# Performance work log

Measured on AMD Instinct MI355X. Metric: run time of the kernel, lower is better.

Reference implementation:

```python
import jax, jax.numpy as jnp
import numpy as np

B, S, E, H = 16, 512, 4096, 8
HD = E // H  # 512, must equal S for this module's math
LN_EPS = 1e-5
NORM_EPS = 1e-12


def setup_inputs() -> dict:
    key = jax.random.key(0)
    ks = jax.random.split(key, 16)
    s_e = 1.0 / np.sqrt(E)
    s_h = 1.0 / np.sqrt(HD)
    return {
        "x": jax.random.normal(ks[0], (B, S, E), jnp.float32),
        "Wq": jax.random.normal(ks[1], (E, E), jnp.float32) * s_e,
        "bq": jnp.zeros((E,), jnp.float32),
        "Wk": jax.random.normal(ks[2], (E, E), jnp.float32) * s_e,
        "bk": jnp.zeros((E,), jnp.float32),
        "Wv": jax.random.normal(ks[3], (E, E), jnp.float32) * s_e,
        "bv": jnp.zeros((E,), jnp.float32),
        "g_q": jnp.ones((HD,), jnp.float32),
        "b_q": jnp.zeros((HD,), jnp.float32),
        "g_k": jnp.ones((HD,), jnp.float32),
        "b_k": jnp.zeros((HD,), jnp.float32),
        "Wg": jax.random.normal(ks[4], (2 * HD, HD), jnp.float32) * s_h,
        "bg": jnp.zeros((2 * HD,), jnp.float32),
        "Wo": jax.random.normal(ks[5], (E, E), jnp.float32) * s_e,
        "bo": jnp.zeros((E,), jnp.float32),
    }


def _layernorm(t, g, b):
    mu = jnp.mean(t, axis=-1, keepdims=True)
    var = jnp.mean(jnp.square(t - mu), axis=-1, keepdims=True)
    return (t - mu) * jax.lax.rsqrt(var + LN_EPS) * g + b


def reference(x, Wq, bq, Wk, bk, Wv, bv, g_q, b_q, g_k, b_k, Wg, bg, Wo, bo):
    # projections + head split: [B,H,S,HD]
    def proj(W, bias):
        y = jnp.einsum('bse,fe->bsf', x, W) + bias
        return y.reshape(B, S, H, HD).transpose(0, 2, 1, 3)

    q = proj(Wq, bq)
    k = proj(Wk, bk)
    v = proj(Wv, bv)

    # per-head QK LayerNorm over head_dim
    q = _layernorm(q, g_q, b_q)
    k = _layernorm(k, g_k, b_k)

    # scores [B,H,S,S]; note S == HD by construction
    scores = jnp.einsum('bhsd,bhtd->bhst', q, k) / np.sqrt(HD)

    # GeGLU over last dim (linear HD -> 2*HD, chunk, gelu gate)
    h = jnp.einsum('bhst,ft->bhsf', scores, Wg) + bg
    val, gate = h[..., :HD], h[..., HD:]
    w = val * jax.nn.gelu(gate, approximate=False)

    # L2 normalize over last dim (torch F.normalize p=2)
    norm = jnp.sqrt(jnp.sum(jnp.square(w), axis=-1, keepdims=True))
    w = w / jnp.maximum(norm, NORM_EPS)

    # attention-value matmul: [B,H,S,HD] x [B,H,S,HD] with HD==S
    out = jnp.einsum('bhst,bhtd->bhsd', w, v)
    out = out.transpose(0, 2, 1, 3).reshape(B, S, E)
    return jnp.einsum('bse,fe->bsf', out, Wo) + bo
```

## Files before the change

### kernel.cpp

```cpp
#include <hip/hip_runtime.h>
#include <math.h>

#define TILE 128
#define BK 64

typedef __bf16 bf16x8 __attribute__((ext_vector_type(8)));
typedef float f32x4 __attribute__((ext_vector_type(4)));
typedef short short8 __attribute__((ext_vector_type(8)));
typedef unsigned int uint2v __attribute__((ext_vector_type(2)));
typedef unsigned int uint4v __attribute__((ext_vector_type(4)));

__device__ __forceinline__ float bf2f(unsigned short u) {
  union { unsigned int i; float f; } v; v.i = ((unsigned int)u) << 16; return v.f;
}
__device__ __forceinline__ unsigned short f2bf(float f) {
  union { float fl; unsigned int i; } v; v.fl = f;
  unsigned int x = v.i;
  return (unsigned short)((x + 0x7FFFu + ((x >> 16) & 1u)) >> 16);
}
__device__ __forceinline__ unsigned int cvt_pk_bf16(float lo, float hi) {
  unsigned int r;
  asm("v_cvt_pk_bf16_f32 %0, %1, %2" : "=v"(r) : "v"(lo), "v"(hi));
  return r;
}
__device__ __forceinline__ void gl_lds16(const unsigned short* g, void* l) {
  __builtin_amdgcn_global_load_lds(
      (const __attribute__((address_space(1))) unsigned int*)g,
      (__attribute__((address_space(3))) unsigned int*)l, 16, 0, 0);
}

template<int CF32, int HAS_BIAS>
__global__ __launch_bounds__(512)
void gemm256(const unsigned short* __restrict__ A,
             const unsigned short* __restrict__ B,
             const float* __restrict__ bias,
             void* __restrict__ Cv,
             int M, int N, int K, int lda, int ldb, int ldc, int nbn)
{
  __shared__ alignas(16) unsigned char LDS[131072];
  const int NT = K >> 6;

  const int nwg = (int)gridDim.x;
  const int bid = (int)blockIdx.x;
  const int swz = (bid & 7) * (nwg >> 3) + (bid >> 3);
  const int tm = (swz / nbn) * 256;
  const int tn = (swz % nbn) * 256;

  const int tid = (int)threadIdx.x;
  const int lane = tid & 63;
  const int wv = tid >> 6;
  const int wm = wv >> 2;
  const int wn = wv & 3;
  const int l16 = lane & 15;
  const int kg = lane >> 4;

  const int srow = tid >> 3;
  const int scolb = ((tid & 7) * 16) ^ (((tid >> 3) & 7) << 4);
  const unsigned short* Abase = A + (long)tm * lda + (scolb >> 1);
  const unsigned short* Bbase = B + (long)tn * ldb + (scolb >> 1);
  const int ldsw = (tid >> 6) * 1024;

  const int colswz0 = (kg * 16) ^ ((l16 & 7) << 4);
  const int colswz1 = (64 + kg * 16) ^ ((l16 & 7) << 4);

  f32x4 acc[8][4];
  #pragma unroll
  for (int i = 0; i < 8; ++i)
    #pragma unroll
    for (int j = 0; j < 4; ++j)
      #pragma unroll
      for (int e = 0; e < 4; ++e) acc[i][j][e] = 0.f;

  auto stageA = [&](int t) {
    const int buf = t & 1;
    #pragma unroll
    for (int h = 0; h < 2; ++h)
      #pragma unroll
      for (int i = 0; i < 2; ++i)
        gl_lds16(Abase + (long)(h * 128 + srow + i * 64) * lda + t * 64,
                 &LDS[buf * 32768 + h * 16384 + i * 8192 + ldsw]);
  };
  auto stageBh = [&](int t, int h) {
    const int buf = t & 1;
    #pragma unroll
    for (int i = 0; i < 2; ++i)
      gl_lds16(Bbase + (long)(h * 128 + srow + i * 64) * ldb + t * 64,
               &LDS[65536 + buf * 32768 + h * 16384 + i * 8192 + ldsw]);
  };

  stageA(0); stageBh(0, 0); stageBh(0, 1);
  stageA(1); stageBh(1, 0); stageBh(1, 1);
  asm volatile("s_waitcnt vmcnt(8)" ::: "memory");
  __builtin_amdgcn_s_barrier();

  for (int t = 0; t < NT; ++t) {
    const unsigned char* aB = &LDS[(t & 1) * 32768 + wm * 16384];
    const unsigned char* bB = &LDS[65536 + (t & 1) * 32768 + (wn >> 1) * 16384];
    const int brow = (wn & 1) * 64;
    bf16x8 bfrag[4][2];
    #pragma unroll
    for (int j = 0; j < 4; ++j) {
      bf16x8 a0k0 = *(const bf16x8*)(aB + ((2 * j + 0) * 16 + l16) * 128 + colswz0);
      bf16x8 a0k1 = *(const bf16x8*)(aB + ((2 * j + 0) * 16 + l16) * 128 + colswz1);
      bf16x8 a1k0 = *(const bf16x8*)(aB + ((2 * j + 1) * 16 + l16) * 128 + colswz0);
      bf16x8 a1k1 = *(const bf16x8*)(aB + ((2 * j + 1) * 16 + l16) * 128 + colswz1);
      if (j == 0) {
        #pragma unroll
        for (int ni = 0; ni < 4; ++ni) {
          bfrag[ni][0] = *(const bf16x8*)(bB + (brow + ni * 16 + l16) * 128 + colswz0);
          bfrag[ni][1] = *(const bf16x8*)(bB + (brow + ni * 16 + l16) * 128 + colswz1);
        }
        if (t > 0 && t + 1 < NT) stageA(t + 1);
      } else if (j == 1) {
        if (t + 2 < NT) stageBh(t + 2, 0);
      } else if (j == 2) {
        if (t + 2 < NT) stageBh(t + 2, 1);
      }
      __builtin_amdgcn_s_barrier();
      asm volatile("s_waitcnt lgkmcnt(0)" ::: "memory");
      __builtin_amdgcn_sched_barrier(0);
      __builtin_amdgcn_s_setprio(1);
      #pragma unroll
      for (int ni = 0; ni < 4; ++ni) {
        acc[2 * j + 0][ni] = __builtin_amdgcn_mfma_f32_16x16x32_bf16(a0k0, bfrag[ni][0], acc[2 * j + 0][ni], 0, 0, 0);
        acc[2 * j + 0][ni] = __builtin_amdgcn_mfma_f32_16x16x32_bf16(a0k1, bfrag[ni][1], acc[2 * j + 0][ni], 0, 0, 0);
        acc[2 * j + 1][ni] = __builtin_amdgcn_mfma_f32_16x16x32_bf16(a1k0, bfrag[ni][0], acc[2 * j + 1][ni], 0, 0, 0);
        acc[2 * j + 1][ni] = __builtin_amdgcn_mfma_f32_16x16x32_bf16(a1k1, bfrag[ni][1], acc[2 * j + 1][ni], 0, 0, 0);
      }
      __builtin_amdgcn_s_setprio(0);
      if (j == 3) {
        if (t >= NT - 2) { asm volatile("s_waitcnt vmcnt(0)" ::: "memory"); }
        else             { asm volatile("s_waitcnt vmcnt(4)" ::: "memory"); }
        __builtin_amdgcn_sched_barrier(0);
      }
      __builtin_amdgcn_s_barrier();
    }
  }

  const int crow0 = tm + wm * 128 + kg * 4;
  const int ccol0 = tn + wn * 64 + l16;
  #pragma unroll
  for (int ni = 0; ni < 4; ++ni) {
    const int col = ccol0 + ni * 16;
    const float bv = HAS_BIAS ? bias[col] : 0.f;
    #pragma unroll
    for (int mi = 0; mi < 8; ++mi) {
      #pragma unroll
      for (int jj = 0; jj < 4; ++jj) {
        const int row = crow0 + mi * 16 + jj;
        const float v = acc[mi][ni][jj] + bv;
        if (CF32) ((float*)Cv)[(long)row * ldc + col] = v;
        else ((unsigned short*)Cv)[(long)row * ldc + col] = f2bf(v);
      }
    }
  }
}

__global__ __launch_bounds__(256)
void cvt_bf16(const float* __restrict__ in, unsigned short* __restrict__ out, long n8)
{
  long i = (long)blockIdx.x * 256 + threadIdx.x;
  const long stride = (long)gridDim.x * 256;
  for (; i < n8; i += stride) {
    f32x4 v0 = *(const f32x4*)(in + i * 8);
    f32x4 v1 = *(const f32x4*)(in + i * 8 + 4);
    uint4v o;
    o[0] = cvt_pk_bf16(v0[0], v0[1]);
    o[1] = cvt_pk_bf16(v0[2], v0[3]);
    o[2] = cvt_pk_bf16(v1[0], v1[1]);
    o[3] = cvt_pk_bf16(v1[2], v1[3]);
    *(uint4v*)(out + i * 8) = o;
  }
}

template<int HAS_BIAS>
__global__ __launch_bounds__(256, 2)
void gemm_bt(const unsigned short* __restrict__ A, const unsigned short* __restrict__ B,
             const float* __restrict__ bias, unsigned short* __restrict__ C,
             int M, int N, int K, int lda, int ldb, int ldc,
             long sAo, long sAi, int nAi,
             long sBo, long sBi, int nBi,
             long sCo, long sCi, int nCi,
             float alpha)
{
  __shared__ alignas(16) unsigned short lA[TILE * BK];
  __shared__ alignas(16) unsigned short lB[TILE * BK];

  const int z = blockIdx.z;
  const unsigned short* Ab = A + (long)(z / nAi) * sAo + (long)(z % nAi) * sAi;
  const unsigned short* Bb = B + (long)(z / nBi) * sBo + (long)(z % nBi) * sBi;
  unsigned short* Cb = C + (long)(z / nCi) * sCo + (long)(z % nCi) * sCi;

  const int tm = blockIdx.y * TILE;
  const int tn = blockIdx.x * TILE;
  const int tid = (int)threadIdx.x;
  const int lane = tid & 63;
  const int wave = tid >> 6;
  const int wm = (wave >> 1) * 64;
  const int wn = (wave & 1) * 64;
  const int l16 = lane & 15;
  const int kg = lane >> 4;

  f32x4 acc[4][4];
  #pragma unroll
  for (int i = 0; i < 4; ++i)
    #pragma unroll
    for (int j = 0; j < 4; ++j)
      #pragma unroll
      for (int e = 0; e < 4; ++e) acc[i][j][e] = 0.f;

  const int srow = tid >> 3;
  const int sc8 = (tid & 7) * 8;
  const int fbA = (wm + l16) * BK + kg * 8;
  const int fbB = (wn + l16) * BK + kg * 8;

  for (int k0 = 0; k0 < K; k0 += BK) {
    short8 ra[4], rb[4];
    #pragma unroll
    for (int i = 0; i < 4; ++i) {
      ra[i] = *(const short8*)(Ab + (long)(tm + srow + i * 32) * lda + k0 + sc8);
      rb[i] = *(const short8*)(Bb + (long)(tn + srow + i * 32) * ldb + k0 + sc8);
    }
    __syncthreads();
    #pragma unroll
    for (int i = 0; i < 4; ++i) {
      *(short8*)&lA[(srow + i * 32) * BK + sc8] = ra[i];
      *(short8*)&lB[(srow + i * 32) * BK + sc8] = rb[i];
    }
    __syncthreads();
    #pragma unroll
    for (int kk = 0; kk < 2; ++kk) {
      bf16x8 af[4], bfr[4];
      #pragma unroll
      for (int mi = 0; mi < 4; ++mi)
        af[mi] = *(const bf16x8*)&lA[fbA + mi * 16 * BK + kk * 32];
      #pragma unroll
      for (int ni = 0; ni < 4; ++ni)
        bfr[ni] = *(const bf16x8*)&lB[fbB + ni * 16 * BK + kk * 32];
      #pragma unroll
      for (int mi = 0; mi < 4; ++mi)
        #pragma unroll
        for (int ni = 0; ni < 4; ++ni)
          acc[mi][ni] = __builtin_amdgcn_mfma_f32_16x16x32_bf16(af[mi], bfr[ni], acc[mi][ni], 0, 0, 0);
    }
  }

  #pragma unroll
  for (int ni = 0; ni < 4; ++ni) {
    int col = tn + wn + ni * 16 + l16;
    float bv = HAS_BIAS ? bias[col] : 0.f;
    #pragma unroll
    for (int mi = 0; mi < 4; ++mi)
      #pragma unroll
      for (int j = 0; j < 4; ++j) {
        int row = tm + wm + mi * 16 + kg * 4 + j;
        Cb[(long)row * ldc + col] = f2bf(acc[mi][ni][j] * alpha + bv);
      }
  }
}

__global__ __launch_bounds__(256)
void ln_rows(unsigned short* __restrict__ t, const float* __restrict__ g,
             const float* __restrict__ b)
{
  const int row = blockIdx.x * 4 + ((int)threadIdx.x >> 6);
  const int lane = (int)threadIdx.x & 63;
  unsigned short* p = t + (long)row * 512 + lane * 8;
  short8 rv = *(const short8*)p;
  float x[8];
  #pragma unroll
  for (int j = 0; j < 8; ++j) x[j] = bf2f((unsigned short)rv[j]);
  float s = 0.f;
  #pragma unroll
  for (int j = 0; j < 8; ++j) s += x[j];
  #pragma unroll
  for (int off = 32; off > 0; off >>= 1) s += __shfl_xor(s, off, 64);
  float mu = s * (1.f / 512.f);
  float vs = 0.f;
  #pragma unroll
  for (int j = 0; j < 8; ++j) { float d = x[j] - mu; vs += d * d; }
  #pragma unroll
  for (int off = 32; off > 0; off >>= 1) vs += __shfl_xor(vs, off, 64);
  float rs = rsqrtf(vs * (1.f / 512.f) + 1e-5f);
  f32x4 gv0 = *(const f32x4*)(g + lane * 8);
  f32x4 gv1 = *(const f32x4*)(g + lane * 8 + 4);
  f32x4 bv0 = *(const f32x4*)(b + lane * 8);
  f32x4 bv1 = *(const f32x4*)(b + lane * 8 + 4);
  short8 ov;
  #pragma unroll
  for (int j = 0; j < 4; ++j) ov[j] = (short)f2bf((x[j] - mu) * rs * gv0[j] + bv0[j]);
  #pragma unroll
  for (int j = 0; j < 4; ++j) ov[4 + j] = (short)f2bf((x[4 + j] - mu) * rs * gv1[j] + bv1[j]);
  *(short8*)p = ov;
}

__global__ __launch_bounds__(256)
void gate_norm(const unsigned short* __restrict__ h, unsigned short* __restrict__ w)
{
  const int row = blockIdx.x * 4 + ((int)threadIdx.x >> 6);
  const int lane = (int)threadIdx.x & 63;
  const unsigned short* hp = h + (long)row * 1024 + lane * 8;
  short8 vv = *(const short8*)hp;
  short8 gg = *(const short8*)(hp + 512);
  float wv[8];
  float ssq = 0.f;
  #pragma unroll
  for (int j = 0; j < 8; ++j) {
    float val = bf2f((unsigned short)vv[j]);
    float gt  = bf2f((unsigned short)gg[j]);
    float tt  = val * (0.5f * gt * (1.f + erff(gt * 0.70710678118654752f)));
    wv[j] = tt;
    ssq += tt * tt;
  }
  #pragma unroll
  for (int off = 32; off > 0; off >>= 1) ssq += __shfl_xor(ssq, off, 64);
  float scale = 1.f / fmaxf(sqrtf(ssq), 1e-12f);
  short8 ov;
  #pragma unroll
  for (int j = 0; j < 8; ++j) ov[j] = (short)f2bf(wv[j] * scale);
  *(short8*)(w + (long)row * 512 + lane * 8) = ov;
}

__global__ __launch_bounds__(256)
void transpose_v(const unsigned short* __restrict__ v, unsigned short* __restrict__ vT)
{
  __shared__ alignas(16) unsigned short lt[64][72];
  const int bh = blockIdx.z;
  const int b = bh >> 3, hh = bh & 7;
  const int d0 = blockIdx.x * 64, t0 = blockIdx.y * 64;
  const int tid = (int)threadIdx.x;
  const unsigned short* src = v + (long)b * (512L * 4096L) + hh * 512;
  #pragma unroll
  for (int it = 0; it < 2; ++it) {
    int ci = it * 256 + tid;
    int r = ci >> 3, c8 = (ci & 7) * 8;
    *(short8*)&lt[r][c8] = *(const short8*)(src + (long)(t0 + r) * 4096 + d0 + c8);
  }
  __syncthreads();
  unsigned short* dst = vT + ((long)bh * 512 + d0) * 512 + t0;
  #pragma unroll
  for (int it = 0; it < 2; ++it) {
    int ci = it * 256 + tid;
    int rr = ci >> 3, c8 = (ci & 7) * 8;
    short8 o;
    #pragma unroll
    for (int j = 0; j < 8; ++j) o[j] = (short)lt[c8 + j][rr];
    *(short8*)(dst + (long)rr * 512 + c8) = o;
  }
}

extern "C" void kernel_launch(void* const* d_in, const int* in_sizes, int n_in,
                              void* d_out, int out_size, void* d_ws, size_t ws_size,
                              hipStream_t stream)
{
  (void)in_sizes; (void)n_in; (void)out_size; (void)ws_size;
  const float* x   = (const float*)d_in[0];
  const float* Wq  = (const float*)d_in[1];
  const float* bq  = (const float*)d_in[2];
  const float* Wk  = (const float*)d_in[3];
  const float* bk  = (const float*)d_in[4];
  const float* Wv  = (const float*)d_in[5];
  const float* bv  = (const float*)d_in[6];
  const float* g_q = (const float*)d_in[7];
  const float* b_q = (const float*)d_in[8];
  const float* g_k = (const float*)d_in[9];
  const float* b_k = (const float*)d_in[10];
  const float* Wg  = (const float*)d_in[11];
  const float* bg  = (const float*)d_in[12];
  const float* Wo  = (const float*)d_in[13];
  const float* bo  = (const float*)d_in[14];
  float* out = (float*)d_out;

  const long NE  = 33554432L;
  const long NE2 = NE / 2;
  unsigned short* ws    = (unsigned short*)d_ws;
  unsigned short* xb    = ws;
  unsigned short* Wslot = ws + NE;
  unsigned short* qbuf  = ws + NE + NE2;
  unsigned short* kbuf  = ws + 2 * NE + NE2;
  unsigned short* vbuf  = ws + 3 * NE + NE2;
  unsigned short* Wob   = ws + 4 * NE + NE2;
  unsigned short* Wgb   = ws + 5 * NE;
  unsigned short* sbuf  = xb;
  unsigned short* vT    = qbuf;
  unsigned short* hbuf  = kbuf;
  unsigned short* wbuf  = xb;
  unsigned short* obuf  = kbuf;

  dim3 blk256(256), blk512(512);
  const float inv_sqrt_hd = 0.044194173824159216f;

  cvt_bf16<<<16384, blk256, 0, stream>>>(x, xb, NE / 8);
  cvt_bf16<<<256, blk256, 0, stream>>>(Wg, Wgb, 524288L / 8);
  cvt_bf16<<<8192, blk256, 0, stream>>>(Wo, Wob, NE2 / 8);

  cvt_bf16<<<8192, blk256, 0, stream>>>(Wq, Wslot, NE2 / 8);
  gemm256<0, 1><<<512, blk512, 0, stream>>>(xb, Wslot, bq, qbuf,
      8192, 4096, 4096, 4096, 4096, 4096, 16);
  cvt_bf16<<<8192, blk256, 0, stream>>>(Wk, Wslot, NE2 / 8);
  gemm256<0, 1><<<512, blk512, 0, stream>>>(xb, Wslot, bk, kbuf,
      8192, 4096, 4096, 4096, 4096, 4096, 16);
  cvt_bf16<<<8192, blk256, 0, stream>>>(Wv, Wslot, NE2 / 8);
  gemm256<0, 1><<<512, blk512, 0, stream>>>(xb, Wslot, bv, vbuf,
      8192, 4096, 4096, 4096, 4096, 4096, 16);

  ln_rows<<<16384, blk256, 0, stream>>>(qbuf, g_q, b_q);
  ln_rows<<<16384, blk256, 0, stream>>>(kbuf, g_k, b_k);

  gemm_bt<0><<<dim3(4, 4, 128), blk256, 0, stream>>>(qbuf, kbuf, nullptr, sbuf,
      512, 512, 512, 4096, 4096, 512,
      2097152L, 512L, 8, 2097152L, 512L, 8, 262144L, 0L, 1, inv_sqrt_hd);

  transpose_v<<<dim3(8, 8, 128), blk256, 0, stream>>>(vbuf, vT);

  gemm_bt<1><<<dim3(8, 4, 128), blk256, 0, stream>>>(sbuf, Wgb, bg, hbuf,
      512, 1024, 512, 512, 512, 1024,
      262144L, 0L, 1, 0L, 0L, 1, 524288L, 0L, 1, 1.f);

  gate_norm<<<16384, blk256, 0, stream>>>(hbuf, wbuf);

  gemm_bt<0><<<dim3(4, 4, 128), blk256, 0, stream>>>(wbuf, vT, nullptr, obuf,
      512, 512, 512, 512, 512, 4096,
      262144L, 0L, 1, 262144L, 0L, 1, 2097152L, 512L, 8, 1.f);

  gemm256<1, 1><<<512, blk512, 0, stream>>>(obuf, Wob, bo, out,
      8192, 4096, 4096, 4096, 4096, 4096, 16);
}
```

Baseline: 1.450 ms.

## Switch big GEMM to 32x32x16 MFMA with 4x4 supertile block swizzle

The 256x256 GEMM used for the QKV and output projections now computes each wave's 128x64 sub-tile with 32x32x16 bf16 MFMA instead of 16x16x32. This doubles work per instruction and reduces LDS fragment reads per FLOP. The K step is split into two half-phases instead of four quarters, and the A refill and both B-half prefetches are regrouped around them. Block-to-tile mapping now groups workgroups into 4x4 supertiles for better L2 reuse, and the unused M/N arguments are dropped. The epilogue is rewritten for the 32x32 accumulator layout, with a risk of higher register pressure from the larger fragments.

```diff
diff --git a/kernel.cpp b/kernel.cpp
--- a/kernel.cpp
+++ b/kernel.cpp
@@ -6,8 +6,8 @@
 
 typedef __bf16 bf16x8 __attribute__((ext_vector_type(8)));
 typedef float f32x4 __attribute__((ext_vector_type(4)));
+typedef float f32x16 __attribute__((ext_vector_type(16)));
 typedef short short8 __attribute__((ext_vector_type(8)));
-typedef unsigned int uint2v __attribute__((ext_vector_type(2)));
 typedef unsigned int uint4v __attribute__((ext_vector_type(4)));
 
 __device__ __forceinline__ float bf2f(unsigned short u) {
@@ -35,41 +35,41 @@
              const unsigned short* __restrict__ B,
              const float* __restrict__ bias,
              void* __restrict__ Cv,
-             int M, int N, int K, int lda, int ldb, int ldc, int nbn)
+             int K, int lda, int ldb, int ldc, int nbn)
 {
   __shared__ alignas(16) unsigned char LDS[131072];
   const int NT = K >> 6;
 
   const int nwg = (int)gridDim.x;
   const int bid = (int)blockIdx.x;
-  const int swz = (bid & 7) * (nwg >> 3) + (bid >> 3);
-  const int tm = (swz / nbn) * 256;
-  const int tn = (swz % nbn) * 256;
+  const int s = (bid & 7) * (nwg >> 3) + (bid >> 3);
+  const int sTile = s >> 4, w = s & 15;
+  const int snb = nbn >> 2;
+  const int tm = ((sTile / snb) * 4 + (w >> 2)) * 256;
+  const int tn = ((sTile % snb) * 4 + (w & 3)) * 256;
 
   const int tid = (int)threadIdx.x;
   const int lane = tid & 63;
   const int wv = tid >> 6;
   const int wm = wv >> 2;
   const int wn = wv & 3;
-  const int l16 = lane & 15;
-  const int kg = lane >> 4;
+  const int l31 = lane & 31;
+  const int hi16 = ((lane >> 5) << 4);
+  const int swz8 = (lane & 7) << 4;
 
   const int srow = tid >> 3;
   const int scolb = ((tid & 7) * 16) ^ (((tid >> 3) & 7) << 4);
   const unsigned short* Abase = A + (long)tm * lda + (scolb >> 1);
   const unsigned short* Bbase = B + (long)tn * ldb + (scolb >> 1);
-  const int ldsw = (tid >> 6) * 1024;
-
-  const int colswz0 = (kg * 16) ^ ((l16 & 7) << 4);
-  const int colswz1 = (64 + kg * 16) ^ ((l16 & 7) << 4);
-
-  f32x4 acc[8][4];
-  #pragma unroll
-  for (int i = 0; i < 8; ++i)
-    #pragma unroll
-    for (int j = 0; j < 4; ++j)
-      #pragma unroll
-      for (int e = 0; e < 4; ++e) acc[i][j][e] = 0.f;
+  const int ldsw = wv * 1024;
+
+  f32x16 acc[4][2];
+  #pragma unroll
+  for (int i = 0; i < 4; ++i)
+    #pragma unroll
+    for (int j = 0; j < 2; ++j)
+      #pragma unroll
+      for (int e = 0; e < 16; ++e) acc[i][j][e] = 0.f;
 
   auto stageA = [&](int t) {
     const int buf = t & 1;
@@ -97,58 +97,71 @@
     const unsigned char* aB = &LDS[(t & 1) * 32768 + wm * 16384];
     const unsigned char* bB = &LDS[65536 + (t & 1) * 32768 + (wn >> 1) * 16384];
     const int brow = (wn & 1) * 64;
-    bf16x8 bfrag[4][2];
-    #pragma unroll
-    for (int j = 0; j < 4; ++j) {
-      bf16x8 a0k0 = *(const bf16x8*)(aB + ((2 * j + 0) * 16 + l16) * 128 + colswz0);
-      bf16x8 a0k1 = *(const bf16x8*)(aB + ((2 * j + 0) * 16 + l16) * 128 + colswz1);
-      bf16x8 a1k0 = *(const bf16x8*)(aB + ((2 * j + 1) * 16 + l16) * 128 + colswz0);
-      bf16x8 a1k1 = *(const bf16x8*)(aB + ((2 * j + 1) * 16 + l16) * 128 + colswz1);
-      if (j == 0) {
+    bf16x8 afr[2][4], bfr[2][4];
+
+    #pragma unroll
+    for (int rb = 0; rb < 2; ++rb)
+      #pragma unroll
+      for (int ks = 0; ks < 4; ++ks)
+        afr[rb][ks] = *(const bf16x8*)(aB + (rb * 32 + l31) * 128 + ((ks * 32 + hi16) ^ swz8));
+    #pragma unroll
+    for (int nb = 0; nb < 2; ++nb)
+      #pragma unroll
+      for (int ks = 0; ks < 4; ++ks)
+        bfr[nb][ks] = *(const bf16x8*)(bB + (brow + nb * 32 + l31) * 128 + ((ks * 32 + hi16) ^ swz8));
+    if (t > 0 && t + 1 < NT) stageA(t + 1);
+    __builtin_amdgcn_s_barrier();
+    asm volatile("s_waitcnt lgkmcnt(0)" ::: "memory");
+    __builtin_amdgcn_sched_barrier(0);
+    __builtin_amdgcn_s_setprio(1);
+    #pragma unroll
+    for (int rb = 0; rb < 2; ++rb)
+      #pragma unroll
+      for (int nb = 0; nb < 2; ++nb)
         #pragma unroll
-        for (int ni = 0; ni < 4; ++ni) {
-          bfrag[ni][0] = *(const bf16x8*)(bB + (brow + ni * 16 + l16) * 128 + colswz0);
-          bfrag[ni][1] = *(const bf16x8*)(bB + (brow + ni * 16 + l16) * 128 + colswz1);
-        }
-        if (t > 0 && t + 1 < NT) stageA(t + 1);
-      } else if (j == 1) {
-        if (t + 2 < NT) stageBh(t + 2, 0);
-      } else if (j == 2) {
-        if (t + 2 < NT) stageBh(t + 2, 1);
-      }
-      __builtin_amdgcn_s_barrier();
-      asm volatile("s_waitcnt lgkmcnt(0)" ::: "memory");
-      __builtin_amdgcn_sched_barrier(0);
-      __builtin_amdgcn_s_setprio(1);
-      #pragma unroll
-      for (int ni = 0; ni < 4; ++ni) {
-        acc[2 * j + 0][ni] = __builtin_amdgcn_mfma_f32_16x16x32_bf16(a0k0, bfrag[ni][0], acc[2 * j + 0][ni], 0, 0, 0);
-        acc[2 * j + 0][ni] = __builtin_amdgcn_mfma_f32_16x16x32_bf16(a0k1, bfrag[ni][1], acc[2 * j + 0][ni], 0, 0, 0);
-        acc[2 * j + 1][ni] = __builtin_amdgcn_mfma_f32_16x16x32_bf16(a1k0, bfrag[ni][0], acc[2 * j + 1][ni], 0, 0, 0);
-        acc[2 * j + 1][ni] = __builtin_amdgcn_mfma_f32_16x16x32_bf16(a1k1, bfrag[ni][1], acc[2 * j + 1][ni], 0, 0, 0);
-      }
-      __builtin_amdgcn_s_setprio(0);
-      if (j == 3) {
-        if (t >= NT - 2) { asm volatile("s_waitcnt vmcnt(0)" ::: "memory"); }
-        else             { asm volatile("s_waitcnt vmcnt(4)" ::: "memory"); }
-        __builtin_amdgcn_sched_barrier(0);
-      }
-      __builtin_amdgcn_s_barrier();
-    }
-  }
-
-  const int crow0 = tm + wm * 128 + kg * 4;
-  const int ccol0 = tn + wn * 64 + l16;
-  #pragma unroll
-  for (int ni = 0; ni < 4; ++ni) {
-    const int col = ccol0 + ni * 16;
+        for (int ks = 0; ks < 4; ++ks)
+          acc[rb][nb] = __builtin_amdgcn_mfma_f32_32x32x16_bf16(
+              afr[rb][ks], bfr[nb][ks], acc[rb][nb], 0, 0, 0);
+    __builtin_amdgcn_s_setprio(0);
+    __builtin_amdgcn_s_barrier();
+
+    #pragma unroll
+    for (int rb = 0; rb < 2; ++rb)
+      #pragma unroll
+      for (int ks = 0; ks < 4; ++ks)
+        afr[rb][ks] = *(const bf16x8*)(aB + ((2 + rb) * 32 + l31) * 128 + ((ks * 32 + hi16) ^ swz8));
+    if (t + 2 < NT) { stageBh(t + 2, 0); stageBh(t + 2, 1); }
+    __builtin_amdgcn_s_barrier();
+    asm volatile("s_waitcnt lgkmcnt(0)" ::: "memory");
+    __builtin_amdgcn_sched_barrier(0);
+    __builtin_amdgcn_s_setprio(1);
+    #pragma unroll
+    for (int rb = 0; rb < 2; ++rb)
+      #pragma unroll
+      for (int nb = 0; nb < 2; ++nb)
+        #pragma unroll
+        for (int ks = 0; ks < 4; ++ks)
+          acc[2 + rb][nb] = __builtin_amdgcn_mfma_f32_32x32x16_bf16(
+              afr[rb][ks], bfr[nb][ks], acc[2 + rb][nb], 0, 0, 0);
+    __builtin_amdgcn_s_setprio(0);
+    if (t >= NT - 2) { asm volatile("s_waitcnt vmcnt(0)" ::: "memory"); }
+    else             { asm volatile("s_waitcnt vmcnt(4)" ::: "memory"); }
+    __builtin_amdgcn_sched_barrier(0);
+    __builtin_amdgcn_s_barrier();
+  }
+
+  const int r0 = tm + wm * 128 + ((lane >> 5) << 2);
+  const int c0 = tn + wn * 64 + l31;
+  #pragma unroll
+  for (int nb = 0; nb < 2; ++nb) {
+    const int col = c0 + nb * 32;
     const float bv = HAS_BIAS ? bias[col] : 0.f;
     #pragma unroll
-    for (int mi = 0; mi < 8; ++mi) {
-      #pragma unroll
-      for (int jj = 0; jj < 4; ++jj) {
-        const int row = crow0 + mi * 16 + jj;
-        const float v = acc[mi][ni][jj] + bv;
+    for (int mi = 0; mi < 4; ++mi) {
+      #pragma unroll
+      for (int r = 0; r < 16; ++r) {
+        const int row = r0 + mi * 32 + (r & 3) + ((r >> 2) << 3);
+        const float v = acc[mi][nb][r] + bv;
         if (CF32) ((float*)Cv)[(long)row * ldc + col] = v;
         else ((unsigned short*)Cv)[(long)row * ldc + col] = f2bf(v);
       }
@@ -396,13 +409,13 @@
 
   cvt_bf16<<<8192, blk256, 0, stream>>>(Wq, Wslot, NE2 / 8);
   gemm256<0, 1><<<512, blk512, 0, stream>>>(xb, Wslot, bq, qbuf,
-      8192, 4096, 4096, 4096, 4096, 4096, 16);
+      4096, 4096, 4096, 4096, 16);
   cvt_bf16<<<8192, blk256, 0, stream>>>(Wk, Wslot, NE2 / 8);
   gemm256<0, 1><<<512, blk512, 0, stream>>>(xb, Wslot, bk, kbuf,
-      8192, 4096, 4096, 4096, 4096, 4096, 16);
+      4096, 4096, 4096, 4096, 16);
   cvt_bf16<<<8192, blk256, 0, stream>>>(Wv, Wslot, NE2 / 8);
   gemm256<0, 1><<<512, blk512, 0, stream>>>(xb, Wslot, bv, vbuf,
-      8192, 4096, 4096, 4096, 4096, 4096, 16);
+      4096, 4096, 4096, 4096, 16);
 
   ln_rows<<<16384, blk256, 0, stream>>>(qbuf, g_q, b_q);
   ln_rows<<<16384, blk256, 0, stream>>>(kbuf, g_k, b_k);
@@ -424,5 +437,5 @@
       262144L, 0L, 1, 262144L, 0L, 1, 2097152L, 512L, 8, 1.f);
 
   gemm256<1, 1><<<512, blk512, 0, stream>>>(obuf, Wob, bo, out,
-      8192, 4096, 4096, 4096, 4096, 4096, 16);
-}
+      4096, 4096, 4096, 4096, 16);
+}
```

After: 1.498 ms. +3.3%, slower.

## Software-pipeline LDS fragment loads across phases and tile 4x4 blocks for L2 locality

Applied to the files above, without the earlier changes.

Reworks the main 256x256 GEMM loop so A fragments for the next phase and B fragments plus the first A fragment for the next K-tile are read from LDS while the current MFMAs run. It uses partial lgkmcnt waits and double-buffered B fragment registers, and unrolls the K loop by two. It also remaps workgroup IDs into 4x4 super-tiles to improve L2 reuse of A and B panels. This costs more VGPRs and more delicate wait/barrier accounting, and assumes NT is even.

```diff
diff --git a/kernel.cpp b/kernel.cpp
--- a/kernel.cpp
+++ b/kernel.cpp
@@ -7,7 +7,6 @@
 typedef __bf16 bf16x8 __attribute__((ext_vector_type(8)));
 typedef float f32x4 __attribute__((ext_vector_type(4)));
 typedef short short8 __attribute__((ext_vector_type(8)));
-typedef unsigned int uint2v __attribute__((ext_vector_type(2)));
 typedef unsigned int uint4v __attribute__((ext_vector_type(4)));
 
 __device__ __forceinline__ float bf2f(unsigned short u) {
@@ -35,16 +34,18 @@
              const unsigned short* __restrict__ B,
              const float* __restrict__ bias,
              void* __restrict__ Cv,
-             int M, int N, int K, int lda, int ldb, int ldc, int nbn)
+             int K, int lda, int ldb, int ldc, int nbn)
 {
   __shared__ alignas(16) unsigned char LDS[131072];
   const int NT = K >> 6;
 
   const int nwg = (int)gridDim.x;
   const int bid = (int)blockIdx.x;
-  const int swz = (bid & 7) * (nwg >> 3) + (bid >> 3);
-  const int tm = (swz / nbn) * 256;
-  const int tn = (swz % nbn) * 256;
+  const int s = (bid & 7) * (nwg >> 3) + (bid >> 3);
+  const int sTile = s >> 4, w = s & 15;
+  const int snb = nbn >> 2;
+  const int tm = ((sTile / snb) * 4 + (w >> 2)) * 256;
+  const int tn = ((sTile % snb) * 4 + (w & 3)) * 256;
 
   const int tid = (int)threadIdx.x;
   const int lane = tid & 63;
@@ -58,10 +59,12 @@
   const int scolb = ((tid & 7) * 16) ^ (((tid >> 3) & 7) << 4);
   const unsigned short* Abase = A + (long)tm * lda + (scolb >> 1);
   const unsigned short* Bbase = B + (long)tn * ldb + (scolb >> 1);
-  const int ldsw = (tid >> 6) * 1024;
+  const int ldsw = wv * 1024;
 
   const int colswz0 = (kg * 16) ^ ((l16 & 7) << 4);
   const int colswz1 = (64 + kg * 16) ^ ((l16 & 7) << 4);
+  const int bq16 = (wn >> 1) * 16384;
+  const int brow = (wn & 1) * 64;
 
   f32x4 acc[8][4];
   #pragma unroll
@@ -71,8 +74,7 @@
       #pragma unroll
       for (int e = 0; e < 4; ++e) acc[i][j][e] = 0.f;
 
-  auto stageA = [&](int t) {
-    const int buf = t & 1;
+  auto stageA = [&](int t, int buf) {
     #pragma unroll
     for (int h = 0; h < 2; ++h)
       #pragma unroll
@@ -80,74 +82,105 @@
         gl_lds16(Abase + (long)(h * 128 + srow + i * 64) * lda + t * 64,
                  &LDS[buf * 32768 + h * 16384 + i * 8192 + ldsw]);
   };
-  auto stageBh = [&](int t, int h) {
-    const int buf = t & 1;
+  auto stageBh = [&](int t, int h, int buf) {
     #pragma unroll
     for (int i = 0; i < 2; ++i)
       gl_lds16(Bbase + (long)(h * 128 + srow + i * 64) * ldb + t * 64,
                &LDS[65536 + buf * 32768 + h * 16384 + i * 8192 + ldsw]);
   };
 
-  stageA(0); stageBh(0, 0); stageBh(0, 1);
-  stageA(1); stageBh(1, 0); stageBh(1, 1);
+  stageA(0, 0); stageBh(0, 0, 0); stageBh(0, 1, 0);
+  stageA(1, 1); stageBh(1, 0, 1); stageBh(1, 1, 1);
   asm volatile("s_waitcnt vmcnt(8)" ::: "memory");
   __builtin_amdgcn_s_barrier();
 
-  for (int t = 0; t < NT; ++t) {
-    const unsigned char* aB = &LDS[(t & 1) * 32768 + wm * 16384];
-    const unsigned char* bB = &LDS[65536 + (t & 1) * 32768 + (wn >> 1) * 16384];
-    const int brow = (wn & 1) * 64;
-    bf16x8 bfrag[4][2];
-    #pragma unroll
-    for (int j = 0; j < 4; ++j) {
-      bf16x8 a0k0 = *(const bf16x8*)(aB + ((2 * j + 0) * 16 + l16) * 128 + colswz0);
-      bf16x8 a0k1 = *(const bf16x8*)(aB + ((2 * j + 0) * 16 + l16) * 128 + colswz1);
-      bf16x8 a1k0 = *(const bf16x8*)(aB + ((2 * j + 1) * 16 + l16) * 128 + colswz0);
-      bf16x8 a1k1 = *(const bf16x8*)(aB + ((2 * j + 1) * 16 + l16) * 128 + colswz1);
-      if (j == 0) {
-        #pragma unroll
-        for (int ni = 0; ni < 4; ++ni) {
-          bfrag[ni][0] = *(const bf16x8*)(bB + (brow + ni * 16 + l16) * 128 + colswz0);
-          bfrag[ni][1] = *(const bf16x8*)(bB + (brow + ni * 16 + l16) * 128 + colswz1);
-        }
-        if (t > 0 && t + 1 < NT) stageA(t + 1);
-      } else if (j == 1) {
-        if (t + 2 < NT) stageBh(t + 2, 0);
-      } else if (j == 2) {
-        if (t + 2 < NT) stageBh(t + 2, 1);
-      }
-      __builtin_amdgcn_s_barrier();
-      asm volatile("s_waitcnt lgkmcnt(0)" ::: "memory");
-      __builtin_amdgcn_sched_barrier(0);
-      __builtin_amdgcn_s_setprio(1);
-      #pragma unroll
-      for (int ni = 0; ni < 4; ++ni) {
-        acc[2 * j + 0][ni] = __builtin_amdgcn_mfma_f32_16x16x32_bf16(a0k0, bfrag[ni][0], acc[2 * j + 0][ni], 0, 0, 0);
-        acc[2 * j + 0][ni] = __builtin_amdgcn_mfma_f32_16x16x32_bf16(a0k1, bfrag[ni][1], acc[2 * j + 0][ni], 0, 0, 0);
-        acc[2 * j + 1][ni] = __builtin_amdgcn_mfma_f32_16x16x32_bf16(a1k0, bfrag[ni][0], acc[2 * j + 1][ni], 0, 0, 0);
-        acc[2 * j + 1][ni] = __builtin_amdgcn_mfma_f32_16x16x32_bf16(a1k1, bfrag[ni][1], acc[2 * j + 1][ni], 0, 0, 0);
-      }
-      __builtin_amdgcn_s_setprio(0);
-      if (j == 3) {
-        if (t >= NT - 2) { asm volatile("s_waitcnt vmcnt(0)" ::: "memory"); }
-        else             { asm volatile("s_waitcnt vmcnt(4)" ::: "memory"); }
-        __builtin_amdgcn_sched_barrier(0);
-      }
-      __builtin_amdgcn_s_barrier();
-    }
-  }
-
-  const int crow0 = tm + wm * 128 + kg * 4;
-  const int ccol0 = tn + wn * 64 + l16;
+  bf16x8 af[2][2][2];
+  bf16x8 bfE[4][2], bfO[4][2];
+
+#define LOADA(P, RB, BASE)                                                     \
+  af[P][0][0] = *(const bf16x8*)((BASE) + ((RB) * 16 + l16) * 128 + colswz0);  \
+  af[P][0][1] = *(const bf16x8*)((BASE) + ((RB) * 16 + l16) * 128 + colswz1);  \
+  af[P][1][0] = *(const bf16x8*)((BASE) + ((RB + 1) * 16 + l16) * 128 + colswz0); \
+  af[P][1][1] = *(const bf16x8*)((BASE) + ((RB + 1) * 16 + l16) * 128 + colswz1);
+
+#define LOADB(BF, BASE)                                                        \
+  _Pragma("unroll")                                                            \
+  for (int ni = 0; ni < 4; ++ni) {                                             \
+    BF[ni][0] = *(const bf16x8*)((BASE) + (brow + ni * 16 + l16) * 128 + colswz0); \
+    BF[ni][1] = *(const bf16x8*)((BASE) + (brow + ni * 16 + l16) * 128 + colswz1); \
+  }
+
+#define MFMA16(R0, P, BF)                                                      \
+  _Pragma("unroll")                                                            \
+  for (int ni = 0; ni < 4; ++ni) {                                             \
+    acc[R0][ni] = __builtin_amdgcn_mfma_f32_16x16x32_bf16(af[P][0][0], BF[ni][0], acc[R0][ni], 0, 0, 0);         \
+    acc[R0][ni] = __builtin_amdgcn_mfma_f32_16x16x32_bf16(af[P][0][1], BF[ni][1], acc[R0][ni], 0, 0, 0);         \
+    acc[R0 + 1][ni] = __builtin_amdgcn_mfma_f32_16x16x32_bf16(af[P][1][0], BF[ni][0], acc[R0 + 1][ni], 0, 0, 0); \
+    acc[R0 + 1][ni] = __builtin_amdgcn_mfma_f32_16x16x32_bf16(af[P][1][1], BF[ni][1], acc[R0 + 1][ni], 0, 0, 0); \
+  }
+
+#define PHASE_STD(P_LOAD, RB_LOAD, R0, P_USE, BF, EXTRA)                       \
+  LOADA(P_LOAD, RB_LOAD, aB)                                                   \
+  EXTRA                                                                        \
+  asm volatile("s_waitcnt lgkmcnt(4)" ::: "memory");                           \
+  __builtin_amdgcn_sched_barrier(0);                                           \
+  __builtin_amdgcn_s_setprio(1);                                               \
+  MFMA16(R0, P_USE, BF)                                                        \
+  __builtin_amdgcn_s_setprio(0);                                               \
+  __builtin_amdgcn_s_barrier();
+
+#define TILE_BODY(TPAR, BFU, BFN)                                              \
+  {                                                                            \
+    const unsigned char* aB  = &LDS[(TPAR) * 32768 + wm * 16384];              \
+    const unsigned char* naB = &LDS[(1 - (TPAR)) * 32768 + wm * 16384];        \
+    const unsigned char* nbB = &LDS[65536 + (1 - (TPAR)) * 32768 + bq16];      \
+    PHASE_STD(1, 2, 0, 0, BFU, )                                               \
+    PHASE_STD(0, 4, 2, 1, BFU,                                                 \
+              if (t > 0 && t + 1 < NT) stageA(t + 1, 1 - (TPAR));)             \
+    PHASE_STD(1, 6, 4, 0, BFU,                                                 \
+              if (t + 2 < NT) { stageBh(t + 2, 0, TPAR); stageBh(t + 2, 1, TPAR); }) \
+    if (t + 1 < NT) {                                                          \
+      if (t >= NT - 2) { asm volatile("s_waitcnt vmcnt(0)" ::: "memory"); }    \
+      else             { asm volatile("s_waitcnt vmcnt(4)" ::: "memory"); }    \
+      __builtin_amdgcn_s_barrier();                                            \
+      LOADB(BFN, nbB)                                                          \
+      LOADA(0, 0, naB)                                                         \
+      asm volatile("s_waitcnt lgkmcnt(12)" ::: "memory");                      \
+    } else {                                                                   \
+      asm volatile("s_waitcnt lgkmcnt(0)" ::: "memory");                       \
+    }                                                                          \
+    __builtin_amdgcn_sched_barrier(0);                                         \
+    __builtin_amdgcn_s_setprio(1);                                             \
+    MFMA16(6, 1, BFU)                                                          \
+    __builtin_amdgcn_s_setprio(0);                                             \
+  }
+
+  {
+    const unsigned char* aB = &LDS[wm * 16384];
+    const unsigned char* bB = &LDS[65536 + bq16];
+    LOADB(bfE, bB)
+    LOADA(0, 0, aB)
+  }
+
+  for (int t2 = 0; t2 < NT; t2 += 2) {
+    { const int t = t2;     TILE_BODY(0, bfE, bfO) }
+    { const int t = t2 + 1; TILE_BODY(1, bfO, bfE) }
+  }
+#undef LOADA
+#undef LOADB
+#undef MFMA16
+#undef PHASE_STD
+#undef TILE_BODY
+
   #pragma unroll
   for (int ni = 0; ni < 4; ++ni) {
-    const int col = ccol0 + ni * 16;
+    const int col = tn + wn * 64 + ni * 16 + l16;
     const float bv = HAS_BIAS ? bias[col] : 0.f;
     #pragma unroll
     for (int mi = 0; mi < 8; ++mi) {
       #pragma unroll
       for (int jj = 0; jj < 4; ++jj) {
-        const int row = crow0 + mi * 16 + jj;
+        const int row = tm + wm * 128 + mi * 16 + kg * 4 + jj;
         const float v = acc[mi][ni][jj] + bv;
         if (CF32) ((float*)Cv)[(long)row * ldc + col] = v;
         else ((unsigned short*)Cv)[(long)row * ldc + col] = f2bf(v);
@@ -396,13 +429,13 @@
 
   cvt_bf16<<<8192, blk256, 0, stream>>>(Wq, Wslot, NE2 / 8);
   gemm256<0, 1><<<512, blk512, 0, stream>>>(xb, Wslot, bq, qbuf,
-      8192, 4096, 4096, 4096, 4096, 4096, 16);
+      4096, 4096, 4096, 4096, 16);
   cvt_bf16<<<8192, blk256, 0, stream>>>(Wk, Wslot, NE2 / 8);
   gemm256<0, 1><<<512, blk512, 0, stream>>>(xb, Wslot, bk, kbuf,
-      8192, 4096, 4096, 4096, 4096, 4096, 16);
+      4096, 4096, 4096, 4096, 16);
   cvt_bf16<<<8192, blk256, 0, stream>>>(Wv, Wslot, NE2 / 8);
   gemm256<0, 1><<<512, blk512, 0, stream>>>(xb, Wslot, bv, vbuf,
-      8192, 4096, 4096, 4096, 4096, 4096, 16);
+      4096, 4096, 4096, 4096, 16);
 
   ln_rows<<<16384, blk256, 0, stream>>>(qbuf, g_q, b_q);
   ln_rows<<<16384, blk256, 0, stream>>>(kbuf, g_k, b_k);
@@ -424,5 +457,5 @@
       262144L, 0L, 1, 262144L, 0L, 1, 2097152L, 512L, 8, 1.f);
 
   gemm256<1, 1><<<512, blk512, 0, stream>>>(obuf, Wob, bo, out,
-      8192, 4096, 4096, 4096, 4096, 4096, 16);
-}
+      4096, 4096, 4096, 4096, 16);
+}
```

Result: slower. 2.840 ms (+95.9%).

## Fuse QKV projections into one GEMM and use 256-tile kernel for batched GEMMs

Applied to the files above, without the earlier changes.

Concatenates Wq/Wk/Wv into one bf16 weight buffer and runs a single 8192x12288 GEMM that routes each output tile to q, k or v with the matching bias. This removes two launches and the serialized per-weight conversions. The 256x256 pipelined gemm256 gains a batched mode and replaces the older 128-tile gemm_bt for the per-head scores, GeGLU and attention-value GEMMs. The non-batched tile mapping also changes to 4x4 supertile grouping for L2 locality. Batched launches have fewer blocks (512-1024) with large tiles, which may underfill the GPU, and the workspace layout is reshuffled to fit the larger weight buffer.

```diff
diff --git a/kernel.cpp b/kernel.cpp
--- a/kernel.cpp
+++ b/kernel.cpp
@@ -1,13 +1,9 @@
 #include <hip/hip_runtime.h>
 #include <math.h>
-
-#define TILE 128
-#define BK 64
 
 typedef __bf16 bf16x8 __attribute__((ext_vector_type(8)));
 typedef float f32x4 __attribute__((ext_vector_type(4)));
 typedef short short8 __attribute__((ext_vector_type(8)));
-typedef unsigned int uint2v __attribute__((ext_vector_type(2)));
 typedef unsigned int uint4v __attribute__((ext_vector_type(4)));
 
 __device__ __forceinline__ float bf2f(unsigned short u) {
@@ -29,22 +25,40 @@
       (__attribute__((address_space(3))) unsigned int*)l, 16, 0, 0);
 }
 
-template<int CF32, int HAS_BIAS>
+template<int BATCH, int SPLIT3, int CF32, int HAS_BIAS>
 __global__ __launch_bounds__(512)
 void gemm256(const unsigned short* __restrict__ A,
              const unsigned short* __restrict__ B,
-             const float* __restrict__ bias,
-             void* __restrict__ Cv,
-             int M, int N, int K, int lda, int ldb, int ldc, int nbn)
+             const float* __restrict__ b0, const float* __restrict__ b1,
+             const float* __restrict__ b2,
+             void* __restrict__ C0, void* __restrict__ C1, void* __restrict__ C2,
+             int K, int lda, int ldb, int ldc, int nbn, float alpha,
+             long sAo, long sAi, int nAi,
+             long sBo, long sBi, int nBi,
+             long sCo, long sCi, int nCi)
 {
   __shared__ alignas(16) unsigned char LDS[131072];
   const int NT = K >> 6;
 
-  const int nwg = (int)gridDim.x;
-  const int bid = (int)blockIdx.x;
-  const int swz = (bid & 7) * (nwg >> 3) + (bid >> 3);
-  const int tm = (swz / nbn) * 256;
-  const int tn = (swz % nbn) * 256;
+  int tm, tn;
+  long offA = 0, offB = 0, offC = 0;
+  if (BATCH) {
+    const int bx = (int)blockIdx.x;
+    tm = (bx / nbn) * 256;
+    tn = (bx % nbn) * 256;
+    const int z = (int)blockIdx.z;
+    offA = (long)(z / nAi) * sAo + (long)(z % nAi) * sAi;
+    offB = (long)(z / nBi) * sBo + (long)(z % nBi) * sBi;
+    offC = (long)(z / nCi) * sCo + (long)(z % nCi) * sCi;
+  } else {
+    const int nwg = (int)gridDim.x;
+    const int bid = (int)blockIdx.x;
+    const int s = (bid & 7) * (nwg >> 3) + (bid >> 3);
+    const int sTile = s >> 4, w = s & 15;
+    const int snb = nbn >> 2;
+    tm = ((sTile / snb) * 4 + (w >> 2)) * 256;
+    tn = ((sTile % snb) * 4 + (w & 3)) * 256;
+  }
 
   const int tid = (int)threadIdx.x;
   const int lane = tid & 63;
@@ -56,9 +70,9 @@
 
   const int srow = tid >> 3;
   const int scolb = ((tid & 7) * 16) ^ (((tid >> 3) & 7) << 4);
-  const unsigned short* Abase = A + (long)tm * lda + (scolb >> 1);
-  const unsigned short* Bbase = B + (long)tn * ldb + (scolb >> 1);
-  const int ldsw = (tid >> 6) * 1024;
+  const unsigned short* Abase = A + offA + (long)tm * lda + (scolb >> 1);
+  const unsigned short* Bbase = B + offB + (long)tn * ldb + (scolb >> 1);
+  const int ldsw = wv * 1024;
 
   const int colswz0 = (kg * 16) ^ ((l16 & 7) << 4);
   const int colswz1 = (64 + kg * 16) ^ ((l16 & 7) << 4);
@@ -137,20 +151,22 @@
     }
   }
 
-  const int crow0 = tm + wm * 128 + kg * 4;
-  const int ccol0 = tn + wn * 64 + l16;
+  const int which = SPLIT3 ? (tn >> 12) : 0;
+  const float* bp = SPLIT3 ? (which == 0 ? b0 : (which == 1 ? b1 : b2)) : b0;
+  void* Cp = SPLIT3 ? (which == 0 ? C0 : (which == 1 ? C1 : C2)) : C0;
+  const int tnn = SPLIT3 ? (tn & 4095) : tn;
   #pragma unroll
   for (int ni = 0; ni < 4; ++ni) {
-    const int col = ccol0 + ni * 16;
-    const float bv = HAS_BIAS ? bias[col] : 0.f;
+    const int col = tnn + wn * 64 + ni * 16 + l16;
+    const float bv = HAS_BIAS ? bp[col] : 0.f;
     #pragma unroll
     for (int mi = 0; mi < 8; ++mi) {
       #pragma unroll
       for (int jj = 0; jj < 4; ++jj) {
-        const int row = crow0 + mi * 16 + jj;
-        const float v = acc[mi][ni][jj] + bv;
-        if (CF32) ((float*)Cv)[(long)row * ldc + col] = v;
-        else ((unsigned short*)Cv)[(long)row * ldc + col] = f2bf(v);
+        const int row = tm + wm * 128 + mi * 16 + kg * 4 + jj;
+        const float v = acc[mi][ni][jj] * alpha + bv;
+        if (CF32) ((float*)Cp)[offC + (long)row * ldc + col] = v;
+        else ((unsigned short*)Cp)[offC + (long)row * ldc + col] = f2bf(v);
       }
     }
   }
@@ -170,92 +186,6 @@
     o[2] = cvt_pk_bf16(v1[0], v1[1]);
     o[3] = cvt_pk_bf16(v1[2], v1[3]);
     *(uint4v*)(out + i * 8) = o;
-  }
-}
-
-template<int HAS_BIAS>
-__global__ __launch_bounds__(256, 2)
-void gemm_bt(const unsigned short* __restrict__ A, const unsigned short* __restrict__ B,
-             const float* __restrict__ bias, unsigned short* __restrict__ C,
-             int M, int N, int K, int lda, int ldb, int ldc,
-             long sAo, long sAi, int nAi,
-             long sBo, long sBi, int nBi,
-             long sCo, long sCi, int nCi,
-             float alpha)
-{
-  __shared__ alignas(16) unsigned short lA[TILE * BK];
-  __shared__ alignas(16) unsigned short lB[TILE * BK];
-
-  const int z = blockIdx.z;
-  const unsigned short* Ab = A + (long)(z / nAi) * sAo + (long)(z % nAi) * sAi;
-  const unsigned short* Bb = B + (long)(z / nBi) * sBo + (long)(z % nBi) * sBi;
-  unsigned short* Cb = C + (long)(z / nCi) * sCo + (long)(z % nCi) * sCi;
-
-  const int tm = blockIdx.y * TILE;
-  const int tn = blockIdx.x * TILE;
-  const int tid = (int)threadIdx.x;
-  const int lane = tid & 63;
-  const int wave = tid >> 6;
-  const int wm = (wave >> 1) * 64;
-  const int wn = (wave & 1) * 64;
-  const int l16 = lane & 15;
-  const int kg = lane >> 4;
-
-  f32x4 acc[4][4];
-  #pragma unroll
-  for (int i = 0; i < 4; ++i)
-    #pragma unroll
-    for (int j = 0; j < 4; ++j)
-      #pragma unroll
-      for (int e = 0; e < 4; ++e) acc[i][j][e] = 0.f;
-
-  const int srow = tid >> 3;
-  const int sc8 = (tid & 7) * 8;
-  const int fbA = (wm + l16) * BK + kg * 8;
-  const int fbB = (wn + l16) * BK + kg * 8;
-
-  for (int k0 = 0; k0 < K; k0 += BK) {
-    short8 ra[4], rb[4];
-    #pragma unroll
-    for (int i = 0; i < 4; ++i) {
-      ra[i] = *(const short8*)(Ab + (long)(tm + srow + i * 32) * lda + k0 + sc8);
-      rb[i] = *(const short8*)(Bb + (long)(tn + srow + i * 32) * ldb + k0 + sc8);
-    }
-    __syncthreads();
-    #pragma unroll
-    for (int i = 0; i < 4; ++i) {
-      *(short8*)&lA[(srow + i * 32) * BK + sc8] = ra[i];
-      *(short8*)&lB[(srow + i * 32) * BK + sc8] = rb[i];
-    }
-    __syncthreads();
-    #pragma unroll
-    for (int kk = 0; kk < 2; ++kk) {
-      bf16x8 af[4], bfr[4];
-      #pragma unroll
-      for (int mi = 0; mi < 4; ++mi)
-        af[mi] = *(const bf16x8*)&lA[fbA + mi * 16 * BK + kk * 32];
-      #pragma unroll
-      for (int ni = 0; ni < 4; ++ni)
-        bfr[ni] = *(const bf16x8*)&lB[fbB + ni * 16 * BK + kk * 32];
-      #pragma unroll
-      for (int mi = 0; mi < 4; ++mi)
-        #pragma unroll
-        for (int ni = 0; ni < 4; ++ni)
-          acc[mi][ni] = __builtin_amdgcn_mfma_f32_16x16x32_bf16(af[mi], bfr[ni], acc[mi][ni], 0, 0, 0);
-    }
-  }
-
-  #pragma unroll
-  for (int ni = 0; ni < 4; ++ni) {
-    int col = tn + wn + ni * 16 + l16;
-    float bv = HAS_BIAS ? bias[col] : 0.f;
-    #pragma unroll
-    for (int mi = 0; mi < 4; ++mi)
-      #pragma unroll
-      for (int j = 0; j < 4; ++j) {
-        int row = tm + wm + mi * 16 + kg * 4 + j;
-        Cb[(long)row * ldc + col] = f2bf(acc[mi][ni][j] * alpha + bv);
-      }
   }
 }
 
@@ -375,12 +305,12 @@
   const long NE2 = NE / 2;
   unsigned short* ws    = (unsigned short*)d_ws;
   unsigned short* xb    = ws;
-  unsigned short* Wslot = ws + NE;
-  unsigned short* qbuf  = ws + NE + NE2;
-  unsigned short* kbuf  = ws + 2 * NE + NE2;
-  unsigned short* vbuf  = ws + 3 * NE + NE2;
-  unsigned short* Wob   = ws + 4 * NE + NE2;
-  unsigned short* Wgb   = ws + 5 * NE;
+  unsigned short* Wqkv  = ws + NE;
+  unsigned short* qbuf  = ws + NE + 3 * NE2;
+  unsigned short* kbuf  = qbuf + NE;
+  unsigned short* vbuf  = kbuf + NE;
+  unsigned short* Wgb   = Wqkv;
+  unsigned short* Wob   = Wqkv + 524288;
   unsigned short* sbuf  = xb;
   unsigned short* vT    = qbuf;
   unsigned short* hbuf  = kbuf;
@@ -388,41 +318,51 @@
   unsigned short* obuf  = kbuf;
 
   dim3 blk256(256), blk512(512);
-  const float inv_sqrt_hd = 0.044194173824159216f;
+  const float isq = 0.044194173824159216f;
 
   cvt_bf16<<<16384, blk256, 0, stream>>>(x, xb, NE / 8);
+  cvt_bf16<<<8192, blk256, 0, stream>>>(Wq, Wqkv, NE2 / 8);
+  cvt_bf16<<<8192, blk256, 0, stream>>>(Wk, Wqkv + NE2, NE2 / 8);
+  cvt_bf16<<<8192, blk256, 0, stream>>>(Wv, Wqkv + 2 * NE2, NE2 / 8);
+
+  gemm256<0, 1, 0, 1><<<1536, blk512, 0, stream>>>(
+      xb, Wqkv, bq, bk, bv, qbuf, kbuf, vbuf,
+      4096, 4096, 4096, 4096, 48, 1.f,
+      0L, 0L, 1, 0L, 0L, 1, 0L, 0L, 1);
+
   cvt_bf16<<<256, blk256, 0, stream>>>(Wg, Wgb, 524288L / 8);
   cvt_bf16<<<8192, blk256, 0, stream>>>(Wo, Wob, NE2 / 8);
 
-  cvt_bf16<<<8192, blk256, 0, stream>>>(Wq, Wslot, NE2 / 8);
-  gemm256<0, 1><<<512, blk512, 0, stream>>>(xb, Wslot, bq, qbuf,
-      8192, 4096, 4096, 4096, 4096, 4096, 16);
-  cvt_bf16<<<8192, blk256, 0, stream>>>(Wk, Wslot, NE2 / 8);
-  gemm256<0, 1><<<512, blk512, 0, stream>>>(xb, Wslot, bk, kbuf,
-      8192, 4096, 4096, 4096, 4096, 4096, 16);
-  cvt_bf16<<<8192, blk256, 0, stream>>>(Wv, Wslot, NE2 / 8);
-  gemm256<0, 1><<<512, blk512, 0, stream>>>(xb, Wslot, bv, vbuf,
-      8192, 4096, 4096, 4096, 4096, 4096, 16);
-
   ln_rows<<<16384, blk256, 0, stream>>>(qbuf, g_q, b_q);
   ln_rows<<<16384, blk256, 0, stream>>>(kbuf, g_k, b_k);
 
-  gemm_bt<0><<<dim3(4, 4, 128), blk256, 0, stream>>>(qbuf, kbuf, nullptr, sbuf,
-      512, 512, 512, 4096, 4096, 512,
-      2097152L, 512L, 8, 2097152L, 512L, 8, 262144L, 0L, 1, inv_sqrt_hd);
+  gemm256<1, 0, 0, 0><<<dim3(4, 1, 128), blk512, 0, stream>>>(
+      qbuf, kbuf, nullptr, nullptr, nullptr, sbuf, nullptr, nullptr,
+      512, 4096, 4096, 512, 2, isq,
+      2097152L, 512L, 8,
+      2097152L, 512L, 8,
+      262144L, 0L, 1);
 
   transpose_v<<<dim3(8, 8, 128), blk256, 0, stream>>>(vbuf, vT);
 
-  gemm_bt<1><<<dim3(8, 4, 128), blk256, 0, stream>>>(sbuf, Wgb, bg, hbuf,
-      512, 1024, 512, 512, 512, 1024,
-      262144L, 0L, 1, 0L, 0L, 1, 524288L, 0L, 1, 1.f);
+  gemm256<1, 0, 0, 1><<<dim3(8, 1, 128), blk512, 0, stream>>>(
+      sbuf, Wgb, bg, nullptr, nullptr, hbuf, nullptr, nullptr,
+      512, 512, 512, 1024, 4, 1.f,
+      262144L, 0L, 1,
+      0L, 0L, 1,
+      524288L, 0L, 1);
 
   gate_norm<<<16384, blk256, 0, stream>>>(hbuf, wbuf);
 
-  gemm_bt<0><<<dim3(4, 4, 128), blk256, 0, stream>>>(wbuf, vT, nullptr, obuf,
-      512, 512, 512, 512, 512, 4096,
-      262144L, 0L, 1, 262144L, 0L, 1, 2097152L, 512L, 8, 1.f);
-
-  gemm256<1, 1><<<512, blk512, 0, stream>>>(obuf, Wob, bo, out,
-      8192, 4096, 4096, 4096, 4096, 4096, 16);
-}
+  gemm256<1, 0, 0, 0><<<dim3(4, 1, 128), blk512, 0, stream>>>(
+      wbuf, vT, nullptr, nullptr, nullptr, obuf, nullptr, nullptr,
+      512, 512, 512, 4096, 2, 1.f,
+      262144L, 0L, 1,
+      262144L, 0L, 1,
+      2097152L, 512L, 8);
+
+  gemm256<0, 0, 1, 1><<<512, blk512, 0, stream>>>(
+      obuf, Wob, bo, nullptr, nullptr, out, nullptr, nullptr,
+      4096, 4096, 4096, 4096, 16, 1.f,
+      0L, 0L, 1, 0L, 0L, 1, 0L, 0L, 1);
+}
```

New measurement: 1.428 ms. No clear change (-1.5%).
